# Kernel optimization log

Measured on AMD Instinct MI355X. Metric: run time of the kernel, lower is better.

Reference implementation:

```python
import jax, jax.numpy as jnp
import numpy as np

N_NODES = 100000
N_EDGES = 1200000
N_GRAPHS = 1000
NUM_SHAPES, NUM_COLORS, NUM_CLASSES = 16, 8, 10


def setup_inputs() -> dict:
    key = jax.random.key(0)
    ks = jax.random.split(key, 12)
    x = jax.random.randint(ks[0], (N_NODES, 2), 0, 8, dtype=jnp.int32)
    edge_index = jax.random.randint(ks[1], (2, N_EDGES), 0, N_NODES, dtype=jnp.int32)
    batch = jnp.sort(jax.random.randint(ks[2], (N_NODES,), 0, N_GRAPHS, dtype=jnp.int32))
    s = 0.05
    params = {
        "shape_emb": jax.random.normal(ks[3], (NUM_SHAPES, 8), jnp.float32) * s,
        "color_emb": jax.random.normal(ks[4], (NUM_COLORS, 8), jnp.float32) * s,
        "W_pre": jax.random.normal(ks[5], (32, 16), jnp.float32) * s,
        "b_pre": jnp.zeros((32,), jnp.float32),
        "W_rel1": jax.random.normal(ks[6], (64, 32), jnp.float32) * s,
        "b_rel1": jnp.zeros((64,), jnp.float32),
        "W_root1": jax.random.normal(ks[7], (64, 32), jnp.float32) * s,
        "W_rel2": jax.random.normal(ks[8], (64, 64), jnp.float32) * s,
        "b_rel2": jnp.zeros((64,), jnp.float32),
        "W_root2": jax.random.normal(ks[9], (64, 64), jnp.float32) * s,
        "W_cls": jax.random.normal(ks[10], (NUM_CLASSES, 64), jnp.float32) * s,
        "b_cls": jnp.zeros((NUM_CLASSES,), jnp.float32),
    }
    return dict(x=x, edge_index=edge_index, batch=batch, num_graphs=N_GRAPHS, **params)


def _graph_conv(h, src, dst, W_rel, b_rel, W_root, n_nodes):
    # PyG GraphConv: out = lin_rel(sum_{j in N(i)} x_j) + lin_root(x_i)
    agg = jax.ops.segment_sum(h[src], dst, num_segments=n_nodes)  # [N, d_in]
    return agg @ W_rel.T + b_rel + h @ W_root.T


def reference(x, edge_index, batch, num_graphs,
              shape_emb, color_emb, W_pre, b_pre,
              W_rel1, b_rel1, W_root1, W_rel2, b_rel2, W_root2,
              W_cls, b_cls):
    n_nodes = x.shape[0]
    src, dst = edge_index[0], edge_index[1]
    h = jnp.concatenate([shape_emb[x[:, 0]], color_emb[x[:, 1]]], axis=1)  # [N, 16]
    h = jax.nn.relu(h @ W_pre.T + b_pre)                                    # [N, 32]
    h = jax.nn.relu(_graph_conv(h, src, dst, W_rel1, b_rel1, W_root1, n_nodes))  # [N, 64]
    h = jax.nn.relu(_graph_conv(h, src, dst, W_rel2, b_rel2, W_root2, n_nodes))  # [N, 64]
    # global mean pool over graphs
    sums = jax.ops.segment_sum(h, batch, num_segments=num_graphs)           # [G, 64]
    counts = jax.ops.segment_sum(jnp.ones((n_nodes,), h.dtype), batch, num_segments=num_graphs)
    pooled = sums / jnp.maximum(counts, 1.0)[:, None]
    return pooled @ W_cls.T + b_cls                                         # [G, num_classes]
```

## Files before the change

### kernel.cpp

```cpp
#include <hip/hip_runtime.h>
#include <hip/hip_bf16.h>


#define NGRAPHS 1000
#define SCAN_CHUNK 4096
#define SRCMASK 0x1FFFF

typedef _Float16 f16x8 __attribute__((ext_vector_type(8)));
typedef float f32x4 __attribute__((ext_vector_type(4)));

__global__ __launch_bounds__(256) void k_hist(const int* __restrict__ dst,
                                              unsigned* __restrict__ hist16,
                                              int* __restrict__ rank, int nE)
{
    int e = blockIdx.x * 256 + threadIdx.x;
    if (e >= nE) return;
    int d = dst[e];
    int sh = (d & 1) * 16;
    unsigned old = atomicAdd(&hist16[d >> 1], 1u << sh);
    rank[e] = (old >> sh) & 0xffff;
}

__device__ __forceinline__ int hval(const unsigned* hist16, int i) {
    return (hist16[i >> 1] >> ((i & 1) * 16)) & 0xffff;
}

__global__ __launch_bounds__(256) void k_scan_part(const unsigned* __restrict__ hist16,
                                                   int* __restrict__ bsum, int n)
{
    __shared__ int s[256];
    int t = threadIdx.x;
    int beg = blockIdx.x * SCAN_CHUNK + t * 16;
    int sum = 0;
#pragma unroll
    for (int q = 0; q < 16; q += 2) {
        int i = beg + q;
        if (i < n) {
            unsigned w = hist16[i >> 1];
            sum += (w & 0xffff);
            if (i + 1 < n) sum += (w >> 16);
        }
    }
    s[t] = sum;
    __syncthreads();
    for (int off = 128; off > 0; off >>= 1) {
        if (t < off) s[t] += s[t + off];
        __syncthreads();
    }
    if (t == 0) bsum[blockIdx.x] = s[0];
}

__global__ __launch_bounds__(64) void k_scan_mid(const int* __restrict__ bsum,
                                                 int* __restrict__ boffs,
                                                 int* __restrict__ row_ptr,
                                                 int B, int n)
{
    if (threadIdx.x == 0) {
        int run = 0;
        for (int b = 0; b < B; ++b) {
            boffs[b] = run;
            run += bsum[b];
        }
        row_ptr[n] = run;
    }
}

__global__ __launch_bounds__(256) void k_scan_apply(const unsigned* __restrict__ hist16,
                                                    const int* __restrict__ boffs,
                                                    int* __restrict__ row_ptr, int n)
{
    __shared__ int s[256];
    int t = threadIdx.x;
    int beg = blockIdx.x * SCAN_CHUNK + t * 16;
    int v[16];
    int sum = 0;
#pragma unroll
    for (int q = 0; q < 16; q += 2) {
        int i = beg + q;
        unsigned w = (i < n) ? hist16[i >> 1] : 0u;
        v[q] = (i < n) ? (int)(w & 0xffff) : 0;
        v[q + 1] = (i + 1 < n) ? (int)(w >> 16) : 0;
        sum += v[q] + v[q + 1];
    }
    s[t] = sum;
    __syncthreads();
    for (int off = 1; off < 256; off <<= 1) {
        int x = (t >= off) ? s[t - off] : 0;
        __syncthreads();
        s[t] += x;
        __syncthreads();
    }
    int base = boffs[blockIdx.x] + ((t == 0) ? 0 : s[t - 1]);
#pragma unroll
    for (int q = 0; q < 16; ++q) {
        int i = beg + q;
        if (i < n) {
            row_ptr[i] = base;
            base += v[q];
        }
    }
}

__global__ __launch_bounds__(256) void k_scatteridx(
    const int* __restrict__ src, const int* __restrict__ dst,
    const int* __restrict__ row_ptr, const int* __restrict__ rank,
    const int* __restrict__ code, int* __restrict__ sorted, int nE)
{
    int e = blockIdx.x * 256 + threadIdx.x;
    if (e >= nE) return;
    int d = dst[e];
    int s = src[e];
    sorted[row_ptr[d] + rank[e]] = (code[s] << 17) | s;
}

__global__ __launch_bounds__(256) void k_pre(
    const int* __restrict__ x,
    const float* __restrict__ shape_emb, const float* __restrict__ color_emb,
    const float* __restrict__ W_pre, const float* __restrict__ b_pre,
    _Float16* __restrict__ h1, int* __restrict__ code, int n)
{
    __shared__ float sW[32 * 16];
    __shared__ float sB[32];
    __shared__ float sSE[16 * 8];
    __shared__ float sCE[8 * 8];
    int t = threadIdx.x;
    for (int i = t; i < 32 * 16; i += 256) sW[i] = W_pre[i];
    if (t < 32) sB[t] = b_pre[t];
    for (int i = t; i < 16 * 8; i += 256) sSE[i] = shape_emb[i];
    if (t < 64) sCE[t] = color_emb[t];
    __syncthreads();

    int i = blockIdx.x * 256 + t;
    if (i >= n) return;
    int s = x[2 * i];
    int c = x[2 * i + 1];
    code[i] = (s << 3) | (c & 7);
    float in[16];
#pragma unroll
    for (int k = 0; k < 8; ++k) in[k] = sSE[s * 8 + k];
#pragma unroll
    for (int k = 0; k < 8; ++k) in[8 + k] = sCE[c * 8 + k];

    float acc[32];
#pragma unroll
    for (int j = 0; j < 32; ++j) acc[j] = sB[j];
#pragma unroll
    for (int k = 0; k < 16; ++k) {
        float v = in[k];
#pragma unroll
        for (int j = 0; j < 32; ++j) acc[j] += sW[j * 16 + k] * v;
    }
#pragma unroll
    for (int g = 0; g < 4; ++g) {
        f16x8 o;
#pragma unroll
        for (int q = 0; q < 8; ++q) o[q] = (_Float16)fmaxf(acc[g * 8 + q], 0.f);
        *(f16x8*)(h1 + (size_t)i * 32 + g * 8) = o;
    }
}

__global__ __launch_bounds__(128) void k_table(
    const float* __restrict__ shape_emb, const float* __restrict__ color_emb,
    const float* __restrict__ W_pre, const float* __restrict__ b_pre,
    _Float16* __restrict__ table)
{
    int c = threadIdx.x;
    int si = c >> 3, ci = c & 7;
    float in[16];
#pragma unroll
    for (int k = 0; k < 8; ++k) in[k] = shape_emb[si * 8 + k];
#pragma unroll
    for (int k = 0; k < 8; ++k) in[8 + k] = color_emb[ci * 8 + k];
    float acc[32];
#pragma unroll
    for (int j = 0; j < 32; ++j) acc[j] = b_pre[j];
#pragma unroll
    for (int k = 0; k < 16; ++k) {
        float v = in[k];
#pragma unroll
        for (int j = 0; j < 32; ++j) acc[j] += W_pre[j * 16 + k] * v;
    }
#pragma unroll
    for (int g = 0; g < 4; ++g) {
        f16x8 o;
#pragma unroll
        for (int q = 0; q < 8; ++q) o[q] = (_Float16)fmaxf(acc[g * 8 + q], 0.f);
        *(f16x8*)(table + (size_t)c * 32 + g * 8) = o;
    }
}

__global__ __launch_bounds__(256) void k_agg1_tab(
    const int* __restrict__ row_ptr, const int* __restrict__ sorted,
    const _Float16* __restrict__ table, _Float16* __restrict__ agg, int n)
{
    __shared__ _Float16 tab[128 * 32];
    int t = threadIdx.x;
    for (int i = t * 8; i < 128 * 32; i += 256 * 8)
        *(f16x8*)(tab + i) = *(const f16x8*)(table + i);
    __syncthreads();

    int tid = blockIdx.x * 256 + t;
    int i = tid >> 2;
    int p = tid & 3;
    if (i >= n) return;
    float a[8] = {0, 0, 0, 0, 0, 0, 0, 0};
    float b[8] = {0, 0, 0, 0, 0, 0, 0, 0};
    int e0 = row_ptr[i], e1 = row_ptr[i + 1];
    const _Float16* tp = tab + p * 8;
    int e = e0;
    for (; e + 2 <= e1; e += 2) {
        int c0 = sorted[e] >> 17;
        int c1 = sorted[e + 1] >> 17;
        f16x8 r0 = *(const f16x8*)(tp + c0 * 32);
        f16x8 r1 = *(const f16x8*)(tp + c1 * 32);
#pragma unroll
        for (int q = 0; q < 8; ++q) { a[q] += (float)r0[q]; b[q] += (float)r1[q]; }
    }
    if (e < e1) {
        int c0 = sorted[e] >> 17;
        f16x8 r0 = *(const f16x8*)(tp + c0 * 32);
#pragma unroll
        for (int q = 0; q < 8; ++q) a[q] += (float)r0[q];
    }
    f16x8 o;
#pragma unroll
    for (int q = 0; q < 8; ++q) o[q] = (_Float16)(a[q] + b[q]);
    *(f16x8*)(agg + (size_t)i * 32 + p * 8) = o;
}

template <int WIDTH, int PARTS>
__global__ __launch_bounds__(256) void k_agg(
    const int* __restrict__ row_ptr, const int* __restrict__ sorted,
    const _Float16* __restrict__ h, _Float16* __restrict__ agg, int n)
{
    int tid = blockIdx.x * 256 + threadIdx.x;
    int i = tid / PARTS;
    int p = tid % PARTS;
    if (i >= n) return;
    float a[8] = {0, 0, 0, 0, 0, 0, 0, 0};
    float b[8] = {0, 0, 0, 0, 0, 0, 0, 0};
    int e0 = row_ptr[i], e1 = row_ptr[i + 1];
    const _Float16* hp = h + p * 8;
    int e = e0;
    for (; e + 4 <= e1; e += 4) {
        int s0 = sorted[e] & SRCMASK;
        int s1 = sorted[e + 1] & SRCMASK;
        int s2 = sorted[e + 2] & SRCMASK;
        int s3 = sorted[e + 3] & SRCMASK;
        f16x8 r0 = *(const f16x8*)(hp + (size_t)s0 * WIDTH);
        f16x8 r1 = *(const f16x8*)(hp + (size_t)s1 * WIDTH);
        f16x8 r2 = *(const f16x8*)(hp + (size_t)s2 * WIDTH);
        f16x8 r3 = *(const f16x8*)(hp + (size_t)s3 * WIDTH);
#pragma unroll
        for (int q = 0; q < 8; ++q) {
            a[q] += (float)r0[q] + (float)r2[q];
            b[q] += (float)r1[q] + (float)r3[q];
        }
    }
    for (; e < e1; ++e) {
        int s0 = sorted[e] & SRCMASK;
        f16x8 r0 = *(const f16x8*)(hp + (size_t)s0 * WIDTH);
#pragma unroll
        for (int q = 0; q < 8; ++q) a[q] += (float)r0[q];
    }
    f16x8 o;
#pragma unroll
    for (int q = 0; q < 8; ++q) o[q] = (_Float16)(a[q] + b[q]);
    *(f16x8*)(agg + (size_t)i * WIDTH + p * 8) = o;
}

template <int WIN>
__global__ __launch_bounds__(256) void k_conv_mfma(
    const _Float16* __restrict__ agg, const _Float16* __restrict__ h,
    const float* __restrict__ W_rel, const float* __restrict__ b_rel,
    const float* __restrict__ W_root, _Float16* __restrict__ out, int n)
{
    constexpr int NK = (2 * WIN) / 32;
    int t = threadIdx.x;
    int lane = t & 63;
    int w = t >> 6;
    int col = lane & 15;
    int krow = lane >> 4;

    f16x8 B[NK][4];
#pragma unroll
    for (int ks = 0; ks < NK; ++ks) {
#pragma unroll
        for (int ct = 0; ct < 4; ++ct) {
            int j = ct * 16 + col;
            int kb = ks * 32 + krow * 8;
            const float* srcw = (ks < NK / 2)
                ? (W_rel + (size_t)j * WIN + kb)
                : (W_root + (size_t)j * WIN + (kb - WIN));
            float4 w0 = *(const float4*)(srcw);
            float4 w1 = *(const float4*)(srcw + 4);
            f16x8 bb;
            bb[0] = (_Float16)w0.x; bb[1] = (_Float16)w0.y;
            bb[2] = (_Float16)w0.z; bb[3] = (_Float16)w0.w;
            bb[4] = (_Float16)w1.x; bb[5] = (_Float16)w1.y;
            bb[6] = (_Float16)w1.z; bb[7] = (_Float16)w1.w;
            B[ks][ct] = bb;
        }
        __builtin_amdgcn_sched_barrier(0);
    }

    float bias[4];
#pragma unroll
    for (int ct = 0; ct < 4; ++ct) bias[ct] = b_rel[ct * 16 + col];

    int nodebase = blockIdx.x * 128 + w * 32;

    f32x4 acc[2][4];
#pragma unroll
    for (int nt = 0; nt < 2; ++nt)
#pragma unroll
        for (int ct = 0; ct < 4; ++ct) acc[nt][ct] = (f32x4){0.f, 0.f, 0.f, 0.f};

#pragma unroll
    for (int ks = 0; ks < NK; ++ks) {
        const _Float16* base = (ks < NK / 2) ? agg : h;
        int koff = ((ks < NK / 2) ? ks : ks - NK / 2) * 32 + krow * 8;
#pragma unroll
        for (int nt = 0; nt < 2; ++nt) {
            int i = nodebase + nt * 16 + col;
            i = min(i, n - 1);
            f16x8 a = *(const f16x8*)(base + (size_t)i * WIN + koff);
#pragma unroll
            for (int ct = 0; ct < 4; ++ct)
                acc[nt][ct] = __builtin_amdgcn_mfma_f32_16x16x32_f16(
                    a, B[ks][ct], acc[nt][ct], 0, 0, 0);
        }
    }

#pragma unroll
    for (int nt = 0; nt < 2; ++nt) {
#pragma unroll
        for (int r = 0; r < 4; ++r) {
            int node = nodebase + nt * 16 + krow * 4 + r;
            if (node < n) {
#pragma unroll
                for (int ct = 0; ct < 4; ++ct) {
                    float v = acc[nt][ct][r] + bias[ct];
                    out[(size_t)node * 64 + ct * 16 + col] = (_Float16)fmaxf(v, 0.f);
                }
            }
        }
    }
}

__global__ __launch_bounds__(256) void k_pool_cls(
    const _Float16* __restrict__ h3, const int* __restrict__ batch,
    const float* __restrict__ W_cls, const float* __restrict__ b_cls,
    float* __restrict__ out, int n)
{
    __shared__ float part[4][64];
    __shared__ float pool[64];
    __shared__ int range[2];
    int g = blockIdx.x;
    int t = threadIdx.x;

    if (t < 2) {
        int key = g + t;
        int lo = 0, hi = n;
        while (lo < hi) {
            int mid = (lo + hi) >> 1;
            if (batch[mid] < key) lo = mid + 1; else hi = mid;
        }
        range[t] = lo;
    }
    __syncthreads();
    int start = range[0], end = range[1];

    int j = t & 63;
    int sub = t >> 6;
    float local = 0.f;
    for (int i = start + sub; i < end; i += 4)
        local += (float)h3[(size_t)i * 64 + j];
    part[sub][j] = local;
    __syncthreads();

    if (t < 64) {
        float cnt = (float)(end - start);
        float inv = 1.0f / fmaxf(cnt, 1.0f);
        pool[t] = (part[0][t] + part[1][t] + part[2][t] + part[3][t]) * inv;
    }
    __syncthreads();

    if (t < 10) {
        float acc = b_cls[t];
#pragma unroll
        for (int k = 0; k < 64; ++k) acc += W_cls[t * 64 + k] * pool[k];
        out[(size_t)g * 10 + t] = acc;
    }
}

extern "C" void kernel_launch(void* const* d_in, const int* in_sizes, int n_in,
                              void* d_out, int out_size, void* d_ws, size_t ws_size,
                              hipStream_t stream)
{
    const int* x        = (const int*)d_in[0];
    const int* ei       = (const int*)d_in[1];
    const int* batch    = (const int*)d_in[2];
    const float* shape_emb = (const float*)d_in[4];
    const float* color_emb = (const float*)d_in[5];
    const float* W_pre   = (const float*)d_in[6];
    const float* b_pre   = (const float*)d_in[7];
    const float* W_rel1  = (const float*)d_in[8];
    const float* b_rel1  = (const float*)d_in[9];
    const float* W_root1 = (const float*)d_in[10];
    const float* W_rel2  = (const float*)d_in[11];
    const float* b_rel2  = (const float*)d_in[12];
    const float* W_root2 = (const float*)d_in[13];
    const float* W_cls   = (const float*)d_in[14];
    const float* b_cls   = (const float*)d_in[15];

    const int n  = in_sizes[0] / 2;
    const int nE = in_sizes[1] / 2;
    const int G  = NGRAPHS;
    const int* src = ei;
    const int* dst = ei + nE;

    _Float16* us = (_Float16*)d_ws;
    _Float16* h1B   = us;
    _Float16* agg1B = us + (size_t)n * 32;
    _Float16* h2B   = us + (size_t)n * 64;
    _Float16* agg2B = us + (size_t)n * 128;
    _Float16* h3B   = us;
    _Float16* tabB  = us + (size_t)n * 192;
    int* ints    = (int*)(tabB + 128 * 32);
    int* code    = ints;
    int* row_ptr = code + n;
    unsigned* hist16 = (unsigned*)(row_ptr + (n + 1));
    int* rank    = (int*)(hist16 + (n / 2 + 1));
    int* sorted  = rank + nE;
    int* bsum    = sorted + nE;
    int* boffs   = bsum + 64;

    const int EB = (nE + 255) / 256;
    const int NB = (n + 255) / 256;
    const int CB = (n + 127) / 128;
    const int SB = (n + SCAN_CHUNK - 1) / SCAN_CHUNK;

    hipMemsetAsync(hist16, 0, (size_t)(n / 2 + 1) * sizeof(unsigned), stream);
    k_pre<<<NB, 256, 0, stream>>>(x, shape_emb, color_emb, W_pre, b_pre, h1B, code, n);
    k_table<<<1, 128, 0, stream>>>(shape_emb, color_emb, W_pre, b_pre, tabB);
    k_hist<<<EB, 256, 0, stream>>>(dst, hist16, rank, nE);
    k_scan_part<<<SB, 256, 0, stream>>>(hist16, bsum, n);
    k_scan_mid<<<1, 64, 0, stream>>>(bsum, boffs, row_ptr, SB, n);
    k_scan_apply<<<SB, 256, 0, stream>>>(hist16, boffs, row_ptr, n);
    k_scatteridx<<<EB, 256, 0, stream>>>(src, dst, row_ptr, rank, code, sorted, nE);

    k_agg1_tab<<<((size_t)n * 4 + 255) / 256, 256, 0, stream>>>(row_ptr, sorted, tabB, agg1B, n);
    k_conv_mfma<32><<<CB, 256, 0, stream>>>(agg1B, h1B, W_rel1, b_rel1, W_root1, h2B, n);
    k_agg<64, 8><<<((size_t)n * 8 + 255) / 256, 256, 0, stream>>>(row_ptr, sorted, h2B, agg2B, n);
    k_conv_mfma<64><<<CB, 256, 0, stream>>>(agg2B, h2B, W_rel2, b_rel2, W_root2, h3B, n);
    k_pool_cls<<<G, 256, 0, stream>>>(h3B, batch, W_cls, b_cls, (float*)d_out, n);
}
```

Measured before the change: 288.2 us.

## Fuse layer-1 table aggregation with MFMA conv and drop per-node pre-MLP kernel

Removes the k_pre kernel and the per-node code array. The scatter kernel now computes each source's code directly from x, and the root term of layer 1 is read from the 128-entry precomputed table. Layer-1 aggregation over the shared-memory table is fused with the MFMA GraphConv, so the agg1 and h1 buffers are never written to or read back from global memory. The fused kernel does its neighbor gather with one thread per node row across 16 lanes, which may balance work worse than the previous 4-way split. It also stores the output as scalar fp16 writes.

```diff
diff --git a/kernel.cpp b/kernel.cpp
--- a/kernel.cpp
+++ b/kernel.cpp
@@ -21,10 +21,6 @@
     rank[e] = (old >> sh) & 0xffff;
 }
 
-__device__ __forceinline__ int hval(const unsigned* hist16, int i) {
-    return (hist16[i >> 1] >> ((i & 1) * 16)) & 0xffff;
-}
-
 __global__ __launch_bounds__(256) void k_scan_part(const unsigned* __restrict__ hist16,
                                                    int* __restrict__ bsum, int n)
 {
@@ -103,60 +99,16 @@
 
 __global__ __launch_bounds__(256) void k_scatteridx(
     const int* __restrict__ src, const int* __restrict__ dst,
-    const int* __restrict__ row_ptr, const int* __restrict__ rank,
-    const int* __restrict__ code, int* __restrict__ sorted, int nE)
+    const int* __restrict__ x, const int* __restrict__ row_ptr,
+    const int* __restrict__ rank, int* __restrict__ sorted, int nE)
 {
     int e = blockIdx.x * 256 + threadIdx.x;
     if (e >= nE) return;
     int d = dst[e];
     int s = src[e];
-    sorted[row_ptr[d] + rank[e]] = (code[s] << 17) | s;
-}
-
-__global__ __launch_bounds__(256) void k_pre(
-    const int* __restrict__ x,
-    const float* __restrict__ shape_emb, const float* __restrict__ color_emb,
-    const float* __restrict__ W_pre, const float* __restrict__ b_pre,
-    _Float16* __restrict__ h1, int* __restrict__ code, int n)
-{
-    __shared__ float sW[32 * 16];
-    __shared__ float sB[32];
-    __shared__ float sSE[16 * 8];
-    __shared__ float sCE[8 * 8];
-    int t = threadIdx.x;
-    for (int i = t; i < 32 * 16; i += 256) sW[i] = W_pre[i];
-    if (t < 32) sB[t] = b_pre[t];
-    for (int i = t; i < 16 * 8; i += 256) sSE[i] = shape_emb[i];
-    if (t < 64) sCE[t] = color_emb[t];
-    __syncthreads();
-
-    int i = blockIdx.x * 256 + t;
-    if (i >= n) return;
-    int s = x[2 * i];
-    int c = x[2 * i + 1];
-    code[i] = (s << 3) | (c & 7);
-    float in[16];
-#pragma unroll
-    for (int k = 0; k < 8; ++k) in[k] = sSE[s * 8 + k];
-#pragma unroll
-    for (int k = 0; k < 8; ++k) in[8 + k] = sCE[c * 8 + k];
-
-    float acc[32];
-#pragma unroll
-    for (int j = 0; j < 32; ++j) acc[j] = sB[j];
-#pragma unroll
-    for (int k = 0; k < 16; ++k) {
-        float v = in[k];
-#pragma unroll
-        for (int j = 0; j < 32; ++j) acc[j] += sW[j * 16 + k] * v;
-    }
-#pragma unroll
-    for (int g = 0; g < 4; ++g) {
-        f16x8 o;
-#pragma unroll
-        for (int q = 0; q < 8; ++q) o[q] = (_Float16)fmaxf(acc[g * 8 + q], 0.f);
-        *(f16x8*)(h1 + (size_t)i * 32 + g * 8) = o;
-    }
+    int2 xv = *(const int2*)(x + 2 * s);
+    int c = (xv.x << 3) | (xv.y & 7);
+    sorted[row_ptr[d] + rank[e]] = (c << 17) | s;
 }
 
 __global__ __launch_bounds__(128) void k_table(
@@ -189,43 +141,108 @@
     }
 }
 
-__global__ __launch_bounds__(256) void k_agg1_tab(
+__global__ __launch_bounds__(256) void k_fused1(
     const int* __restrict__ row_ptr, const int* __restrict__ sorted,
-    const _Float16* __restrict__ table, _Float16* __restrict__ agg, int n)
+    const int* __restrict__ x, const _Float16* __restrict__ table,
+    const float* __restrict__ W_rel, const float* __restrict__ b_rel,
+    const float* __restrict__ W_root, _Float16* __restrict__ out, int n)
 {
     __shared__ _Float16 tab[128 * 32];
     int t = threadIdx.x;
-    for (int i = t * 8; i < 128 * 32; i += 256 * 8)
+    for (int i = t * 8; i < 128 * 32; i += 2048)
         *(f16x8*)(tab + i) = *(const f16x8*)(table + i);
-    __syncthreads();
-
-    int tid = blockIdx.x * 256 + t;
-    int i = tid >> 2;
-    int p = tid & 3;
-    if (i >= n) return;
-    float a[8] = {0, 0, 0, 0, 0, 0, 0, 0};
-    float b[8] = {0, 0, 0, 0, 0, 0, 0, 0};
-    int e0 = row_ptr[i], e1 = row_ptr[i + 1];
-    const _Float16* tp = tab + p * 8;
-    int e = e0;
-    for (; e + 2 <= e1; e += 2) {
-        int c0 = sorted[e] >> 17;
-        int c1 = sorted[e + 1] >> 17;
-        f16x8 r0 = *(const f16x8*)(tp + c0 * 32);
-        f16x8 r1 = *(const f16x8*)(tp + c1 * 32);
-#pragma unroll
-        for (int q = 0; q < 8; ++q) { a[q] += (float)r0[q]; b[q] += (float)r1[q]; }
-    }
-    if (e < e1) {
-        int c0 = sorted[e] >> 17;
-        f16x8 r0 = *(const f16x8*)(tp + c0 * 32);
-#pragma unroll
-        for (int q = 0; q < 8; ++q) a[q] += (float)r0[q];
-    }
-    f16x8 o;
-#pragma unroll
-    for (int q = 0; q < 8; ++q) o[q] = (_Float16)(a[q] + b[q]);
-    *(f16x8*)(agg + (size_t)i * 32 + p * 8) = o;
+
+    int lane = t & 63;
+    int w = t >> 6;
+    int col = lane & 15;
+    int krow = lane >> 4;
+
+    f16x8 B[2][4];
+#pragma unroll
+    for (int ks = 0; ks < 2; ++ks) {
+#pragma unroll
+        for (int ct = 0; ct < 4; ++ct) {
+            int j = ct * 16 + col;
+            const float* srcw = (ks == 0 ? W_rel : W_root) + (size_t)j * 32 + krow * 8;
+            float4 w0 = *(const float4*)(srcw);
+            float4 w1 = *(const float4*)(srcw + 4);
+            f16x8 bb;
+            bb[0] = (_Float16)w0.x; bb[1] = (_Float16)w0.y;
+            bb[2] = (_Float16)w0.z; bb[3] = (_Float16)w0.w;
+            bb[4] = (_Float16)w1.x; bb[5] = (_Float16)w1.y;
+            bb[6] = (_Float16)w1.z; bb[7] = (_Float16)w1.w;
+            B[ks][ct] = bb;
+        }
+        __builtin_amdgcn_sched_barrier(0);
+    }
+    float bias[4];
+#pragma unroll
+    for (int ct = 0; ct < 4; ++ct) bias[ct] = b_rel[ct * 16 + col];
+
+    __syncthreads();
+
+    int nodebase = blockIdx.x * 128 + w * 32;
+    f32x4 acc[2][4];
+#pragma unroll
+    for (int nt = 0; nt < 2; ++nt)
+#pragma unroll
+        for (int ct = 0; ct < 4; ++ct) acc[nt][ct] = (f32x4){0.f, 0.f, 0.f, 0.f};
+
+#pragma unroll
+    for (int nt = 0; nt < 2; ++nt) {
+        int i = nodebase + nt * 16 + col;
+        int iC = min(i, n - 1);
+        int e0 = row_ptr[iC];
+        int e1 = (i < n) ? row_ptr[iC + 1] : e0;
+
+        float a[8] = {0, 0, 0, 0, 0, 0, 0, 0};
+        int e = e0;
+        for (; e + 2 <= e1; e += 2) {
+            int c0 = sorted[e] >> 17;
+            int c1 = sorted[e + 1] >> 17;
+            f16x8 r0 = *(const f16x8*)(tab + c0 * 32 + krow * 8);
+            f16x8 r1 = *(const f16x8*)(tab + c1 * 32 + krow * 8);
+#pragma unroll
+            for (int q = 0; q < 8; ++q) a[q] += (float)r0[q] + (float)r1[q];
+        }
+        if (e < e1) {
+            int c0 = sorted[e] >> 17;
+            f16x8 r0 = *(const f16x8*)(tab + c0 * 32 + krow * 8);
+#pragma unroll
+            for (int q = 0; q < 8; ++q) a[q] += (float)r0[q];
+        }
+        f16x8 Aagg;
+#pragma unroll
+        for (int q = 0; q < 8; ++q) Aagg[q] = (_Float16)a[q];
+
+        int2 xv = *(const int2*)(x + 2 * (size_t)iC);
+        int code = (xv.x << 3) | (xv.y & 7);
+        f16x8 Aroot = *(const f16x8*)(tab + code * 32 + krow * 8);
+
+#pragma unroll
+        for (int ct = 0; ct < 4; ++ct)
+            acc[nt][ct] = __builtin_amdgcn_mfma_f32_16x16x32_f16(
+                Aagg, B[0][ct], acc[nt][ct], 0, 0, 0);
+#pragma unroll
+        for (int ct = 0; ct < 4; ++ct)
+            acc[nt][ct] = __builtin_amdgcn_mfma_f32_16x16x32_f16(
+                Aroot, B[1][ct], acc[nt][ct], 0, 0, 0);
+    }
+
+#pragma unroll
+    for (int nt = 0; nt < 2; ++nt) {
+#pragma unroll
+        for (int r = 0; r < 4; ++r) {
+            int node = nodebase + nt * 16 + krow * 4 + r;
+            if (node < n) {
+#pragma unroll
+                for (int ct = 0; ct < 4; ++ct) {
+                    float v = acc[nt][ct][r] + bias[ct];
+                    out[(size_t)node * 64 + ct * 16 + col] = (_Float16)fmaxf(v, 0.f);
+                }
+            }
+        }
+    }
 }
 
 template <int WIDTH, int PARTS>
@@ -421,15 +438,12 @@
     const int* dst = ei + nE;
 
     _Float16* us = (_Float16*)d_ws;
-    _Float16* h1B   = us;
-    _Float16* agg1B = us + (size_t)n * 32;
-    _Float16* h2B   = us + (size_t)n * 64;
-    _Float16* agg2B = us + (size_t)n * 128;
-    _Float16* h3B   = us;
+    _Float16* h2B   = us;
+    _Float16* agg2B = us + (size_t)n * 64;
+    _Float16* h3B   = us + (size_t)n * 128;
     _Float16* tabB  = us + (size_t)n * 192;
     int* ints    = (int*)(tabB + 128 * 32);
-    int* code    = ints;
-    int* row_ptr = code + n;
+    int* row_ptr = ints;
     unsigned* hist16 = (unsigned*)(row_ptr + (n + 1));
     int* rank    = (int*)(hist16 + (n / 2 + 1));
     int* sorted  = rank + nE;
@@ -437,21 +451,19 @@
     int* boffs   = bsum + 64;
 
     const int EB = (nE + 255) / 256;
-    const int NB = (n + 255) / 256;
     const int CB = (n + 127) / 128;
     const int SB = (n + SCAN_CHUNK - 1) / SCAN_CHUNK;
 
     hipMemsetAsync(hist16, 0, (size_t)(n / 2 + 1) * sizeof(unsigned), stream);
-    k_pre<<<NB, 256, 0, stream>>>(x, shape_emb, color_emb, W_pre, b_pre, h1B, code, n);
     k_table<<<1, 128, 0, stream>>>(shape_emb, color_emb, W_pre, b_pre, tabB);
     k_hist<<<EB, 256, 0, stream>>>(dst, hist16, rank, nE);
     k_scan_part<<<SB, 256, 0, stream>>>(hist16, bsum, n);
     k_scan_mid<<<1, 64, 0, stream>>>(bsum, boffs, row_ptr, SB, n);
     k_scan_apply<<<SB, 256, 0, stream>>>(hist16, boffs, row_ptr, n);
-    k_scatteridx<<<EB, 256, 0, stream>>>(src, dst, row_ptr, rank, code, sorted, nE);
-
-    k_agg1_tab<<<((size_t)n * 4 + 255) / 256, 256, 0, stream>>>(row_ptr, sorted, tabB, agg1B, n);
-    k_conv_mfma<32><<<CB, 256, 0, stream>>>(agg1B, h1B, W_rel1, b_rel1, W_root1, h2B, n);
+    k_scatteridx<<<EB, 256, 0, stream>>>(src, dst, x, row_ptr, rank, sorted, nE);
+
+    k_fused1<<<CB, 256, 0, stream>>>(row_ptr, sorted, x, tabB,
+                                     W_rel1, b_rel1, W_root1, h2B, n);
     k_agg<64, 8><<<((size_t)n * 8 + 255) / 256, 256, 0, stream>>>(row_ptr, sorted, h2B, agg2B, n);
     k_conv_mfma<64><<<CB, 256, 0, stream>>>(agg2B, h2B, W_rel2, b_rel2, W_root2, h3B, n);
     k_pool_cls<<<G, 256, 0, stream>>>(h3B, batch, W_cls, b_cls, (float*)d_out, n);
```

Result: faster. 279.7 us (-3.0%).
